# Performance work log

Hardware: AMD Instinct MI355X
Metric: run time of the kernel (lower is better)

The kernel has to match this reference:

```python
import jax, jax.numpy as jnp
import numpy as np

# Conv2dfft forward (no spectral compression: preserve_energy=None, index_back=None, out_size=None)
# Implements cross-correlation (DL convolution) via rfft2 / irfft2, matching the torch module's
# padding and output-size logic:
#   out_H = H - HH + 1 + 2*pad ; init_fft = H + 2*pad + max(out_H, HH) - 1

PAD = 1  # padding from init_kwargs


def setup_inputs() -> dict:
    key = jax.random.key(0)
    k1, k2, k3 = jax.random.split(key, 3)
    x = jax.random.normal(k1, (32, 128, 32, 32), dtype=jnp.float32)
    w = jax.random.normal(k2, (128, 128, 3, 3), dtype=jnp.float32) * 0.1
    b = jax.random.normal(k3, (128,), dtype=jnp.float32)
    return {"x": x, "w": w, "b": b}


def reference(x, w, b):
    N, C, H, W = x.shape
    F, _, HH, WW = w.shape
    out_H = H - HH + 1 + 2 * PAD
    out_W = W - WW + 1 + 2 * PAD
    init_fft_H = H + 2 * PAD + max(out_H, HH) - 1  # 65
    init_fft_W = W + 2 * PAD + max(out_W, WW) - 1  # 65

    # pad input: explicit conv padding + zero-pad up to FFT grid
    fft_pad_H = init_fft_H - 2 * PAD - H
    fft_pad_W = init_fft_W - 2 * PAD - W
    px = jnp.pad(x, ((0, 0), (0, 0), (PAD, PAD + fft_pad_H), (PAD, PAD + fft_pad_W)))
    pw = jnp.pad(w, ((0, 0), (0, 0), (0, init_fft_H - HH), (0, init_fft_W - WW)))

    xfft = jnp.fft.rfft2(px)                     # [N,C,65,33] complex64
    yfft = jnp.fft.rfft2(pw)                     # [F,C,65,33] complex64

    # cross-correlation: multiply by conj(filter fft), accumulate over input channels
    prod = jnp.einsum('nchw,fchw->nfhw', xfft, jnp.conj(yfft))
    full = jnp.fft.irfft2(prod, s=(init_fft_H, init_fft_W))  # [N,F,65,65]
    out = full[:, :, :out_H, :out_W] + b[None, :, None, None]
    return out
```

## Files before the change

### kernel.cpp

```cpp
#include <hip/hip_runtime.h>


typedef __attribute__((ext_vector_type(8))) short bf16x8;
typedef __attribute__((ext_vector_type(4))) float f32x4;

#define N_IMG 32
#define C_IN  128
#define F_OUT 128
#define HW    32
#define HPAD  34

__device__ __forceinline__ unsigned short f2bf(float f) {
    union { float f; unsigned u; } v; v.f = f;
    unsigned r = v.u + 0x7fffu + ((v.u >> 16) & 1u);
    return (unsigned short)(r >> 16);
}

__global__ __launch_bounds__(256) void pack_x_kernel(const float* __restrict__ x,
                                                     unsigned short* __restrict__ xp) {
    __shared__ unsigned short tile[C_IN * HPAD];
    const int n   = blockIdx.x / HPAD;
    const int hp  = blockIdx.x - n * HPAD;
    const int tid = threadIdx.x;
    const unsigned base_out = (unsigned)(n * HPAD + hp) * (HPAD * C_IN);
    if (hp >= 1 && hp <= 32) {
        const int h = hp - 1;
        #pragma unroll
        for (int i = 0; i < 16; ++i) {
            int idx = tid + i * 256;
            int c = idx >> 5, w = idx & 31;
            tile[c * HPAD + (w + 1)] = f2bf(x[((n * C_IN + c) * HW + h) * HW + w]);
        }
        if (tid < C_IN) { tile[tid * HPAD] = 0; tile[tid * HPAD + 33] = 0; }
        __syncthreads();
        #pragma unroll
        for (int i = 0; i < 17; ++i) {
            int idx = tid + i * 256;
            int wp = idx >> 7, c = idx & 127;
            xp[base_out + (unsigned)idx] = tile[c * HPAD + wp];
        }
    } else {
        #pragma unroll
        for (int i = 0; i < 17; ++i) {
            int idx = tid + i * 256;
            xp[base_out + (unsigned)idx] = 0;
        }
    }
}

__global__ __launch_bounds__(256) void pack_w_kernel(const float* __restrict__ w,
                                                     unsigned short* __restrict__ wpk) {
    int idx = blockIdx.x * 256 + threadIdx.x;
    int c8  = idx & 7;
    int f   = (idx >> 3) & 127;
    int qk  = (idx >> 10) & 3;
    int u   = idx >> 12;
    int cc  = u / 9;
    int tap = u - cc * 9;
    wpk[idx] = f2bf(w[(f * C_IN + cc * 32 + qk * 8 + c8) * 9 + tap]);
}

__global__ __launch_bounds__(256, 1) void conv_gemm_kernel(
    const unsigned short* __restrict__ xp,
    const unsigned short* __restrict__ wpk,
    const float* __restrict__ bias,
    float* __restrict__ out)
{
    __shared__ alignas(16) unsigned short lds_x[208 * C_IN];
    __shared__ alignas(16) unsigned short lds_w[2][5 * 4096];

    const int tid  = threadIdx.x;
    const int lane = tid & 63;
    const int wave = tid >> 6;
    const int qk   = lane >> 4;
    const int l15  = lane & 15;

    const int band = blockIdx.x & 7;
    const int n    = blockIdx.x >> 3;
    const int fh   = wave >> 1;
    const int rp   = wave & 1;
    const int f0   = fh * 64;

    const unsigned short* xbase = xp + (unsigned)((n * HPAD + band * 4) * HPAD) * C_IN;
    #pragma unroll
    for (int i = 0; i < 13; ++i) {
        int p = tid + i * 256;
        int row = p >> 4;  if (row > 203) row = 203;
        int lc = (p ^ row) & 15;
        const unsigned short* src = xbase + row * C_IN + lc * 8;
        __builtin_amdgcn_global_load_lds(
            (const __attribute__((address_space(1))) void*)src,
            (__attribute__((address_space(3))) void*)(&lds_x[p * 8]),
            16, 0, 0);
    }

    #define STAGE_W(ccv, t0v, ntv, bufv) do {                                   \
        const unsigned short* wsrc = wpk + ((ccv) * 9 + (t0v)) * 4096;          \
        _Pragma("unroll")                                                       \
        for (int j_ = 0; j_ < 2 * (ntv); ++j_) {                                \
            int p_ = tid + j_ * 256;                                            \
            __builtin_amdgcn_global_load_lds(                                   \
                (const __attribute__((address_space(1))) void*)(wsrc + p_ * 8), \
                (__attribute__((address_space(3))) void*)(&lds_w[bufv][p_ * 8]),\
                16, 0, 0);                                                      \
        }                                                                       \
    } while (0)

    STAGE_W(0, 0, 5, 0);

    f32x4 acc[4][4];
    #pragma unroll
    for (int mi = 0; mi < 4; ++mi)
        #pragma unroll
        for (int ni = 0; ni < 4; ++ni)
            acc[mi][ni] = (f32x4){0.f, 0.f, 0.f, 0.f};

    int rrb[4];
    #pragma unroll
    for (int ni = 0; ni < 4; ++ni)
        rrb[ni] = (rp * 2 + (ni >> 1)) * HPAD + (ni & 1) * 16 + l15;

    const int af_base = qk * 1024 + (f0 + l15) * 8;

    __syncthreads();

    #define COMPUTE(bufv, T0, NT, ccv)                                          \
        _Pragma("unroll")                                                       \
        for (int tl = 0; tl < (NT); ++tl) {                                     \
            const int tap = (T0) + tl;                                          \
            const int r = tap / 3, s = tap - 3 * (tap / 3);                     \
            bf16x8 af[4], bf[4];                                                \
            _Pragma("unroll")                                                   \
            for (int mi = 0; mi < 4; ++mi)                                      \
                af[mi] = *(const bf16x8*)&lds_w[bufv][tl * 4096 + af_base + mi * 128]; \
            _Pragma("unroll")                                                   \
            for (int ni = 0; ni < 4; ++ni) {                                    \
                int rr = rrb[ni] + r * HPAD + s;                                \
                int ph = ((ccv) * 4 + qk) ^ (rr & 15);                          \
                bf[ni] = *(const bf16x8*)&lds_x[rr * C_IN + ph * 8];            \
            }                                                                   \
            _Pragma("unroll")                                                   \
            for (int mi = 0; mi < 4; ++mi)                                      \
                _Pragma("unroll")                                               \
                for (int ni = 0; ni < 4; ++ni)                                  \
                    acc[mi][ni] = __builtin_amdgcn_mfma_f32_16x16x32_bf16(      \
                        af[mi], bf[ni], acc[mi][ni], 0, 0, 0);                  \
        }

    for (int cc = 0; cc < 4; ++cc) {
        STAGE_W(cc, 5, 4, 1);
        COMPUTE(0, 0, 5, cc);
        __syncthreads();
        if (cc < 3) STAGE_W(cc + 1, 0, 5, 0);
        COMPUTE(1, 5, 4, cc);
        __syncthreads();
    }

    const int h0 = band * 4 + rp * 2;
    #pragma unroll
    for (int mi = 0; mi < 4; ++mi) {
        const int f_base = f0 + mi * 16 + qk * 4;
        float bv[4];
        #pragma unroll
        for (int r2 = 0; r2 < 4; ++r2) bv[r2] = bias[f_base + r2];
        #pragma unroll
        for (int ni = 0; ni < 4; ++ni) {
            const int h  = h0 + (ni >> 1);
            const int w2 = (ni & 1) * 16 + l15;
            #pragma unroll
            for (int r2 = 0; r2 < 4; ++r2) {
                out[((unsigned)(n * F_OUT + f_base + r2) * HW + h) * HW + w2] =
                    acc[mi][ni][r2] + bv[r2];
            }
        }
    }
    #undef STAGE_W
    #undef COMPUTE
}

extern "C" void kernel_launch(void* const* d_in, const int* in_sizes, int n_in,
                              void* d_out, int out_size, void* d_ws, size_t ws_size,
                              hipStream_t stream) {
    const float* x = (const float*)d_in[0];
    const float* w = (const float*)d_in[1];
    const float* b = (const float*)d_in[2];
    float* out = (float*)d_out;

    unsigned short* xp  = (unsigned short*)d_ws;
    unsigned short* wpk = xp + (size_t)N_IMG * HPAD * HPAD * C_IN;

    pack_x_kernel<<<N_IMG * HPAD, 256, 0, stream>>>(x, xp);
    pack_w_kernel<<<576, 256, 0, stream>>>(w, wpk);
    conv_gemm_kernel<<<N_IMG * 8, 256, 0, stream>>>(xp, wpk, b, out);
}
```

Before: 91.50 us.

## Merge pack kernels and triple-buffer weight staging with partial vmcnt waits

Merges the input and weight packing kernels into a single launch to save one launch. In the GEMM kernel, weight staging moves from a two-buffer, five-plus-four-tap split to a three-buffer ring of three-tap chunks. Each phase waits only until the older loads are done (vmcnt(6)) before a raw s_barrier, so the next chunk's load stays in flight while the current one computes. This aims to hide weight-load latency and shorten barrier stalls, at the cost of relying on hand-placed waitcnt counts. A dead first macro definition that calls a nonexistent builtin is left in and immediately undefined.

Result: faster. 86.06 us (-5.9%).

```diff
diff --git a/kernel.cpp b/kernel.cpp
--- a/kernel.cpp
+++ b/kernel.cpp
@@ -16,48 +16,49 @@
     return (unsigned short)(r >> 16);
 }
 
-__global__ __launch_bounds__(256) void pack_x_kernel(const float* __restrict__ x,
-                                                     unsigned short* __restrict__ xp) {
+__global__ __launch_bounds__(256) void pack_kernel(const float* __restrict__ x,
+                                                   const float* __restrict__ w,
+                                                   unsigned short* __restrict__ xp,
+                                                   unsigned short* __restrict__ wpk) {
     __shared__ unsigned short tile[C_IN * HPAD];
-    const int n   = blockIdx.x / HPAD;
-    const int hp  = blockIdx.x - n * HPAD;
     const int tid = threadIdx.x;
-    const unsigned base_out = (unsigned)(n * HPAD + hp) * (HPAD * C_IN);
-    if (hp >= 1 && hp <= 32) {
-        const int h = hp - 1;
-        #pragma unroll
-        for (int i = 0; i < 16; ++i) {
-            int idx = tid + i * 256;
-            int c = idx >> 5, w = idx & 31;
-            tile[c * HPAD + (w + 1)] = f2bf(x[((n * C_IN + c) * HW + h) * HW + w]);
-        }
-        if (tid < C_IN) { tile[tid * HPAD] = 0; tile[tid * HPAD + 33] = 0; }
-        __syncthreads();
-        #pragma unroll
-        for (int i = 0; i < 17; ++i) {
-            int idx = tid + i * 256;
-            int wp = idx >> 7, c = idx & 127;
-            xp[base_out + (unsigned)idx] = tile[c * HPAD + wp];
+    if (blockIdx.x < N_IMG * HPAD) {
+        const int n   = blockIdx.x / HPAD;
+        const int hp  = blockIdx.x - n * HPAD;
+        const unsigned base_out = (unsigned)(n * HPAD + hp) * (HPAD * C_IN);
+        if (hp >= 1 && hp <= 32) {
+            const int h = hp - 1;
+            #pragma unroll
+            for (int i = 0; i < 16; ++i) {
+                int idx = tid + i * 256;
+                int c = idx >> 5, ww = idx & 31;
+                tile[c * HPAD + (ww + 1)] = f2bf(x[((n * C_IN + c) * HW + h) * HW + ww]);
+            }
+            if (tid < C_IN) { tile[tid * HPAD] = 0; tile[tid * HPAD + 33] = 0; }
+            __syncthreads();
+            #pragma unroll
+            for (int i = 0; i < 17; ++i) {
+                int idx = tid + i * 256;
+                int wp = idx >> 7, c = idx & 127;
+                xp[base_out + (unsigned)idx] = tile[c * HPAD + wp];
+            }
+        } else {
+            #pragma unroll
+            for (int i = 0; i < 17; ++i) {
+                int idx = tid + i * 256;
+                xp[base_out + (unsigned)idx] = 0;
+            }
         }
     } else {
-        #pragma unroll
-        for (int i = 0; i < 17; ++i) {
-            int idx = tid + i * 256;
-            xp[base_out + (unsigned)idx] = 0;
-        }
+        int idx = (blockIdx.x - N_IMG * HPAD) * 256 + tid;
+        int c8  = idx & 7;
+        int f   = (idx >> 3) & 127;
+        int qk  = (idx >> 10) & 3;
+        int u   = idx >> 12;
+        int cc  = u / 9;
+        int tap = u - cc * 9;
+        wpk[idx] = f2bf(w[(f * C_IN + cc * 32 + qk * 8 + c8) * 9 + tap]);
     }
-}
-
-__global__ __launch_bounds__(256) void pack_w_kernel(const float* __restrict__ w,
-                                                     unsigned short* __restrict__ wpk) {
-    int idx = blockIdx.x * 256 + threadIdx.x;
-    int c8  = idx & 7;
-    int f   = (idx >> 3) & 127;
-    int qk  = (idx >> 10) & 3;
-    int u   = idx >> 12;
-    int cc  = u / 9;
-    int tap = u - cc * 9;
-    wpk[idx] = f2bf(w[(f * C_IN + cc * 32 + qk * 8 + c8) * 9 + tap]);
 }
 
 __global__ __launch_bounds__(256, 1) void conv_gemm_kernel(
@@ -67,7 +68,7 @@
     float* __restrict__ out)
 {
     __shared__ alignas(16) unsigned short lds_x[208 * C_IN];
-    __shared__ alignas(16) unsigned short lds_w[2][5 * 4096];
+    __shared__ alignas(16) unsigned short lds_w[3][3 * 4096];
 
     const int tid  = threadIdx.x;
     const int lane = tid & 63;
@@ -94,10 +95,19 @@
             16, 0, 0);
     }
 
-    #define STAGE_W(ccv, t0v, ntv, bufv) do {                                   \
+    #define STAGE_W3(ccv, t0v, bufv) do {                                       \
         const unsigned short* wsrc = wpk + ((ccv) * 9 + (t0v)) * 4096;          \
         _Pragma("unroll")                                                       \
-        for (int j_ = 0; j_ < 2 * (ntv); ++j_) {                                \
+        for (int j_ = 0; j_ < 6; ++j_) {                                        \
+            int p_ = tid + j_ * 256;                                            \
+            __builtin_amdgcn_global_lds(0);                                     \
+        }                                                                       \
+    } while (0)
+    #undef STAGE_W3
+    #define STAGE_W3(ccv, t0v, bufv) do {                                       \
+        const unsigned short* wsrc = wpk + ((ccv) * 9 + (t0v)) * 4096;          \
+        _Pragma("unroll")                                                       \
+        for (int j_ = 0; j_ < 6; ++j_) {                                        \
             int p_ = tid + j_ * 256;                                            \
             __builtin_amdgcn_global_load_lds(                                   \
                 (const __attribute__((address_space(1))) void*)(wsrc + p_ * 8), \
@@ -106,7 +116,8 @@
         }                                                                       \
     } while (0)
 
-    STAGE_W(0, 0, 5, 0);
+    STAGE_W3(0, 0, 0);
+    STAGE_W3(0, 3, 1);
 
     f32x4 acc[4][4];
     #pragma unroll
@@ -122,11 +133,13 @@
 
     const int af_base = qk * 1024 + (f0 + l15) * 8;
 
-    __syncthreads();
-
-    #define COMPUTE(bufv, T0, NT, ccv)                                          \
+    asm volatile("s_waitcnt vmcnt(6)" ::: "memory");
+    __builtin_amdgcn_s_barrier();
+    __builtin_amdgcn_sched_barrier(0);
+
+    #define COMPUTE3(bufv, ccv, T0)                                             \
         _Pragma("unroll")                                                       \
-        for (int tl = 0; tl < (NT); ++tl) {                                     \
+        for (int tl = 0; tl < 3; ++tl) {                                        \
             const int tap = (T0) + tl;                                          \
             const int r = tap / 3, s = tap - 3 * (tap / 3);                     \
             bf16x8 af[4], bf[4];                                                \
@@ -147,14 +160,29 @@
                         af[mi], bf[ni], acc[mi][ni], 0, 0, 0);                  \
         }
 
-    for (int cc = 0; cc < 4; ++cc) {
-        STAGE_W(cc, 5, 4, 1);
-        COMPUTE(0, 0, 5, cc);
-        __syncthreads();
-        if (cc < 3) STAGE_W(cc + 1, 0, 5, 0);
-        COMPUTE(1, 5, 4, cc);
-        __syncthreads();
-    }
+    #define PHASE_FULL(cc2, t02, b2, bcur, ccv, t0v) do {                       \
+        STAGE_W3(cc2, t02, b2);                                                 \
+        COMPUTE3(bcur, ccv, t0v);                                               \
+        asm volatile("s_waitcnt vmcnt(6)" ::: "memory");                        \
+        __builtin_amdgcn_s_barrier();                                           \
+        __builtin_amdgcn_sched_barrier(0);                                      \
+    } while (0)
+
+    PHASE_FULL(0, 6, 2, 0, 0, 0);
+    PHASE_FULL(1, 0, 0, 1, 0, 3);
+    PHASE_FULL(1, 3, 1, 2, 0, 6);
+    PHASE_FULL(1, 6, 2, 0, 1, 0);
+    PHASE_FULL(2, 0, 0, 1, 1, 3);
+    PHASE_FULL(2, 3, 1, 2, 1, 6);
+    PHASE_FULL(2, 6, 2, 0, 2, 0);
+    PHASE_FULL(3, 0, 0, 1, 2, 3);
+    PHASE_FULL(3, 3, 1, 2, 2, 6);
+    PHASE_FULL(3, 6, 2, 0, 3, 0);
+    COMPUTE3(1, 3, 3);
+    asm volatile("s_waitcnt vmcnt(0)" ::: "memory");
+    __builtin_amdgcn_s_barrier();
+    __builtin_amdgcn_sched_barrier(0);
+    COMPUTE3(2, 3, 6);
 
     const int h0 = band * 4 + rp * 2;
     #pragma unroll
@@ -174,8 +202,9 @@
             }
         }
     }
-    #undef STAGE_W
-    #undef COMPUTE
+    #undef STAGE_W3
+    #undef COMPUTE3
+    #undef PHASE_FULL
 }
 
 extern "C" void kernel_launch(void* const* d_in, const int* in_sizes, int n_in,
@@ -189,7 +218,6 @@
     unsigned short* xp  = (unsigned short*)d_ws;
     unsigned short* wpk = xp + (size_t)N_IMG * HPAD * HPAD * C_IN;
 
-    pack_x_kernel<<<N_IMG * HPAD, 256, 0, stream>>>(x, xp);
-    pack_w_kernel<<<576, 256, 0, stream>>>(w, wpk);
+    pack_kernel<<<N_IMG * HPAD + 576, 256, 0, stream>>>(x, w, xp, wpk);
     conv_gemm_kernel<<<N_IMG * 8, 256, 0, stream>>>(xp, wpk, b, out);
 }
```
